# Kernel tuning notes

Hardware: AMD Instinct MI355X
Metric: run time of the kernel (lower is better)

Reference implementation:

```python
import jax, jax.numpy as jnp
import numpy as np

B, S, E, FF, Q = 8, 2048, 768, 3072, 8  # batch, seq, embed_dim, ffn_dim, n_qubits


def setup_inputs() -> dict:
    key = jax.random.key(0)
    k_x, k_phi, k_w1, k_w2 = jax.random.split(key, 4)
    x = jax.random.normal(k_x, (B, S, E), dtype=jnp.float32)
    # trainable RY angles (one per qubit), like tq.RY(has_params=True)
    phi = jax.random.normal(k_phi, (Q,), dtype=jnp.float32)
    # linear1: n_qubits -> ffn_dim ; linear2: ffn_dim -> embed_dim (torch layout [out, in])
    w1 = jax.random.normal(k_w1, (FF, Q), dtype=jnp.float32) / np.sqrt(Q).astype(np.float32)
    b1 = jnp.zeros((FF,), dtype=jnp.float32)
    w2 = jax.random.normal(k_w2, (E, FF), dtype=jnp.float32) / np.sqrt(FF).astype(np.float32)
    b2 = jnp.zeros((E,), dtype=jnp.float32)
    return {"x": x, "phi": phi, "w1": w1, "b1": b1, "w2": w2, "b2": b2}


def reference(x, phi, w1, b1, w2, b2):
    # Quantum block (exact closed form): for each token, encoder applies
    # RY(x_i) on wire i, then a trainable RY(phi_i) on wire i. Starting from
    # |0>^Q this is a product state; RY compose additively and
    # <Z> after RY(theta)|0> == cos(theta). MeasureAll(PauliZ) therefore gives:
    n_qubits = phi.shape[0]
    meas = jnp.cos(x[..., :n_qubits] + phi)          # [B, S, Q]
    # dropout is identity in eval mode
    h = jax.nn.relu(jnp.einsum('bsq,fq->bsf', meas, w1) + b1)  # [B, S, FF]
    return jnp.einsum('bsf,ef->bse', h, w2) + b2               # [B, S, E]
```

## Files before the change

kernel.cpp:

```cpp
#include <hip/hip_runtime.h>
#include <hip/hip_bf16.h>
#include <stdint.h>

#define M_TOK 16384
#define E_DIM 768
#define FF_DIM 3072
#define Q_N 8

typedef __attribute__((ext_vector_type(8))) short bf16x8;
typedef __attribute__((ext_vector_type(4))) float f32x4;

__device__ inline unsigned short f2bf(float f) {
  union { float f; unsigned u; } v; v.f = f;
  unsigned r = v.u + 0x7fffu + ((v.u >> 16) & 1u);
  return (unsigned short)(r >> 16);
}

__global__ __launch_bounds__(256) void cvt_w2(const float* __restrict__ w2,
                                              __hip_bfloat16* __restrict__ w2b) {
  int i = (blockIdx.x * 256 + threadIdx.x) * 4;
  const int n = E_DIM * FF_DIM;
  if (i < n) {
    float4 v = *(const float4*)(w2 + i);
    ushort4 o;
    o.x = f2bf(v.x); o.y = f2bf(v.y); o.z = f2bf(v.z); o.w = f2bf(v.w);
    *(ushort4*)((unsigned short*)w2b + i) = o;
  }
}

__global__ __launch_bounds__(256) void compute_h(const float* __restrict__ x,
                                                 const float* __restrict__ phi,
                                                 const float* __restrict__ w1,
                                                 const float* __restrict__ b1,
                                                 __hip_bfloat16* __restrict__ hout) {
  __shared__ float s_meas[32][8];
  const int t = threadIdx.x;
  const int bm = blockIdx.x / 6;
  const int bf = blockIdx.x % 6;
  const int m0 = bm * 32;
  const int f0 = bf * 512;

  if (t < 64) {
    int m = t >> 1, hh = t & 1;
    float4 v = *(const float4*)(x + (size_t)(m0 + m) * E_DIM + hh * 4);
    float4 p = *(const float4*)(phi + hh * 4);
    s_meas[m][hh * 4 + 0] = __cosf(v.x + p.x);
    s_meas[m][hh * 4 + 1] = __cosf(v.y + p.y);
    s_meas[m][hh * 4 + 2] = __cosf(v.z + p.z);
    s_meas[m][hh * 4 + 3] = __cosf(v.w + p.w);
  }
  __syncthreads();

  const float4* wr = (const float4*)(w1 + (size_t)(f0 + 2 * t) * Q_N);
  float4 a0 = wr[0], a1 = wr[1], b0 = wr[2], b1v = wr[3];
  float wA[8] = {a0.x, a0.y, a0.z, a0.w, a1.x, a1.y, a1.z, a1.w};
  float wB[8] = {b0.x, b0.y, b0.z, b0.w, b1v.x, b1v.y, b1v.z, b1v.w};
  const float biasA = b1[f0 + 2 * t];
  const float biasB = b1[f0 + 2 * t + 1];

  uint32_t* dst32 = (uint32_t*)hout;
  for (int m = 0; m < 32; ++m) {
    float a = biasA, b = biasB;
#pragma unroll
    for (int q = 0; q < 8; ++q) {
      float mv = s_meas[m][q];
      a = fmaf(mv, wA[q], a);
      b = fmaf(mv, wB[q], b);
    }
    a = fmaxf(a, 0.f);
    b = fmaxf(b, 0.f);
    uint32_t pack = (uint32_t)f2bf(a) | ((uint32_t)f2bf(b) << 16);
    dst32[(size_t)(m0 + m) * (FF_DIM / 2) + (f0 / 2) + t] = pack;
  }
}

#define GLDS16(g, l)                                                          \
  __builtin_amdgcn_global_load_lds(                                           \
      (const __attribute__((address_space(1))) void*)(g),                     \
      (__attribute__((address_space(3))) void*)(l), 16, 0, 0)

#define BUF_ELEMS 28672
#define B_OFF 16384

__global__ __launch_bounds__(512, 1) void gemm_bt(const __hip_bfloat16* __restrict__ A,
                                                  const __hip_bfloat16* __restrict__ Bw,
                                                  const float* __restrict__ b2,
                                                  float* __restrict__ C) {
  const int K = FF_DIM;
  const int N = E_DIM;

  __shared__ __align__(16) __hip_bfloat16 lds[2 * BUF_ELEMS];

  const int t = threadIdx.x;
  const int swz = (blockIdx.x & 7) * 32 + (blockIdx.x >> 3);
  const int bm = swz >> 2;
  const int bn = swz & 3;
  const size_t m0 = (size_t)bm * 256;
  const int n0 = bn * 192;

  const int w = t >> 6, l = t & 63;
  const int wr = w >> 2;
  const int wc = w & 3;
  const int lr = l & 15;
  const int lk = l >> 4;

  const int x0 = lk ^ (lr & 7);
  const int x1 = x0 ^ 4;
  const int baseA = (wr * 128 + lr) * 64;
  const int baseB = B_OFF + (wc * 48 + lr) * 64;
  const int offA0 = baseA + x0 * 8, offA1 = baseA + x1 * 8;
  const int offB0 = baseB + x0 * 8, offB1 = baseB + x1 * 8;

  const int rs = t >> 3;
  const int lc = (t & 7) ^ (rs & 7);
  const __hip_bfloat16* sA[4];
  const __hip_bfloat16* sB[3];
#pragma unroll
  for (int s = 0; s < 4; ++s) sA[s] = A + (m0 + s * 64 + rs) * (size_t)K + lc * 8;
#pragma unroll
  for (int s = 0; s < 3; ++s) sB[s] = Bw + ((size_t)n0 + s * 64 + rs) * K + lc * 8;

  f32x4 acc[8][3] = {};

#define S_EARLY(K0S, WBUF)                                                    \
  {                                                                           \
    __hip_bfloat16* ld = lds + (WBUF) * BUF_ELEMS + t * 8;                    \
    GLDS16(sB[0] + (K0S), ld + 16384);                                        \
    GLDS16(sB[1] + (K0S), ld + 20480);                                        \
    GLDS16(sB[2] + (K0S), ld + 24576);                                        \
    GLDS16(sA[0] + (K0S), ld);                                                \
    GLDS16(sA[2] + (K0S), ld + 8192);                                         \
  }
#define S_LATE(K0S, WBUF)                                                     \
  {                                                                           \
    __hip_bfloat16* ld = lds + (WBUF) * BUF_ELEMS + t * 8;                    \
    GLDS16(sA[1] + (K0S), ld + 4096);                                         \
    GLDS16(sA[3] + (K0S), ld + 12288);                                        \
  }

#define TILE(KT, RBUF, DO_STAGE)                                              \
  {                                                                           \
    const __hip_bfloat16* la = lds + (RBUF) * BUF_ELEMS;                      \
    if (DO_STAGE) S_EARLY(((KT) + 1) * 64, (RBUF) ^ 1);                       \
    bf16x8 af0[4], af1[4], bfx0[3], bfx1[3];                                  \
    _Pragma("unroll") for (int mi = 0; mi < 4; ++mi) {                        \
      af0[mi] = *(const bf16x8*)(la + offA0 + mi * 1024);                     \
      af1[mi] = *(const bf16x8*)(la + offA1 + mi * 1024);                     \
    }                                                                         \
    _Pragma("unroll") for (int ni = 0; ni < 3; ++ni) {                        \
      bfx0[ni] = *(const bf16x8*)(la + offB0 + ni * 1024);                    \
      bfx1[ni] = *(const bf16x8*)(la + offB1 + ni * 1024);                    \
    }                                                                         \
    __builtin_amdgcn_s_setprio(1);                                            \
    _Pragma("unroll") for (int mi = 0; mi < 4; ++mi)                          \
      _Pragma("unroll") for (int ni = 0; ni < 3; ++ni)                        \
        acc[mi][ni] = __builtin_amdgcn_mfma_f32_16x16x32_bf16(                \
            af0[mi], bfx0[ni], acc[mi][ni], 0, 0, 0);                         \
    _Pragma("unroll") for (int mi = 0; mi < 4; ++mi)                          \
      _Pragma("unroll") for (int ni = 0; ni < 3; ++ni)                        \
        acc[mi][ni] = __builtin_amdgcn_mfma_f32_16x16x32_bf16(                \
            af1[mi], bfx1[ni], acc[mi][ni], 0, 0, 0);                         \
    __builtin_amdgcn_s_setprio(0);                                            \
    if (DO_STAGE) {                                                           \
      asm volatile("s_waitcnt vmcnt(5)" ::: "memory");   \
    } else {                                                                  \
      asm volatile("s_waitcnt vmcnt(0)" ::: "memory");                        \
    }                                                                         \
    __builtin_amdgcn_s_barrier();                                             \
    bf16x8 ag0[4], ag1[4];                                                    \
    _Pragma("unroll") for (int mi = 0; mi < 4; ++mi) {                        \
      ag0[mi] = *(const bf16x8*)(la + offA0 + (mi + 4) * 1024);               \
      ag1[mi] = *(const bf16x8*)(la + offA1 + (mi + 4) * 1024);               \
    }                                                                         \
    if (DO_STAGE) S_LATE(((KT) + 1) * 64, (RBUF) ^ 1);                        \
    __builtin_amdgcn_s_setprio(1);                                            \
    _Pragma("unroll") for (int mi = 0; mi < 4; ++mi)                          \
      _Pragma("unroll") for (int ni = 0; ni < 3; ++ni)                        \
        acc[mi + 4][ni] = __builtin_amdgcn_mfma_f32_16x16x32_bf16(            \
            ag0[mi], bfx0[ni], acc[mi + 4][ni], 0, 0, 0);                     \
    _Pragma("unroll") for (int mi = 0; mi < 4; ++mi)                          \
      _Pragma("unroll") for (int ni = 0; ni < 3; ++ni)                        \
        acc[mi + 4][ni] = __builtin_amdgcn_mfma_f32_16x16x32_bf16(            \
            ag1[mi], bfx1[ni], acc[mi + 4][ni], 0, 0, 0);                     \
    __builtin_amdgcn_s_setprio(0);                                            \
    if (DO_STAGE) {                                                           \
      asm volatile("s_waitcnt vmcnt(2)" ::: "memory");  \
      __builtin_amdgcn_s_barrier();                                           \
    }                                                                         \
  }

  S_EARLY(0, 0);
  S_LATE(0, 0);
  asm volatile("s_waitcnt vmcnt(2)" ::: "memory");
  __builtin_amdgcn_s_barrier();

#pragma unroll 1
  for (int tt = 0; tt < 46; tt += 2) {
    TILE(tt + 0, 0, 1);
    TILE(tt + 1, 1, 1);
  }
  TILE(46, 0, 1);
  TILE(47, 1, 0);

#undef TILE
#undef S_EARLY
#undef S_LATE

#pragma unroll
  for (int mi = 0; mi < 8; ++mi) {
    const size_t row = m0 + wr * 128 + mi * 16 + lk * 4;
#pragma unroll
    for (int ni = 0; ni < 3; ++ni) {
      const int col = n0 + wc * 48 + ni * 16 + lr;
      const float bias = b2[col];
#pragma unroll
      for (int rr = 0; rr < 4; ++rr) {
        C[(row + rr) * N + col] = acc[mi][ni][rr] + bias;
      }
    }
  }
}

__global__ __launch_bounds__(256) void fallback_fused(const float* __restrict__ x,
                                                      const float* __restrict__ phi,
                                                      const float* __restrict__ w1,
                                                      const float* __restrict__ b1,
                                                      const float* __restrict__ w2,
                                                      const float* __restrict__ b2,
                                                      float* __restrict__ out) {
  __shared__ float s_h[FF_DIM];
  __shared__ float s_meas[Q_N];
  const int t = threadIdx.x;
  const size_t m = blockIdx.x;
  if (t < Q_N) s_meas[t] = __cosf(x[m * E_DIM + t] + phi[t]);
  __syncthreads();
  for (int f = t; f < FF_DIM; f += 256) {
    const float4* wr = (const float4*)(w1 + (size_t)f * Q_N);
    float4 a = wr[0], b = wr[1];
    float acc = b1[f];
    acc = fmaf(s_meas[0], a.x, acc); acc = fmaf(s_meas[1], a.y, acc);
    acc = fmaf(s_meas[2], a.z, acc); acc = fmaf(s_meas[3], a.w, acc);
    acc = fmaf(s_meas[4], b.x, acc); acc = fmaf(s_meas[5], b.y, acc);
    acc = fmaf(s_meas[6], b.z, acc); acc = fmaf(s_meas[7], b.w, acc);
    s_h[f] = fmaxf(acc, 0.f);
  }
  __syncthreads();
  for (int e = t; e < E_DIM; e += 256) {
    const float* w2r = w2 + (size_t)e * FF_DIM;
    float acc = b2[e];
    for (int f = 0; f < FF_DIM; f += 4) {
      float4 wv = *(const float4*)(w2r + f);
      acc = fmaf(s_h[f + 0], wv.x, acc);
      acc = fmaf(s_h[f + 1], wv.y, acc);
      acc = fmaf(s_h[f + 2], wv.z, acc);
      acc = fmaf(s_h[f + 3], wv.w, acc);
    }
    out[m * E_DIM + e] = acc;
  }
}

extern "C" void kernel_launch(void* const* d_in, const int* in_sizes, int n_in,
                              void* d_out, int out_size, void* d_ws, size_t ws_size,
                              hipStream_t stream) {
  const float* x   = (const float*)d_in[0];
  const float* phi = (const float*)d_in[1];
  const float* w1  = (const float*)d_in[2];
  const float* b1  = (const float*)d_in[3];
  const float* w2  = (const float*)d_in[4];
  const float* b2  = (const float*)d_in[5];
  float* out = (float*)d_out;

  const size_t H_BYTES   = (size_t)M_TOK * FF_DIM * 2;
  const size_t W2B_BYTES = (size_t)E_DIM * FF_DIM * 2;
  const size_t NEED = H_BYTES + W2B_BYTES;

  if (ws_size >= NEED) {
    __hip_bfloat16* h   = (__hip_bfloat16*)d_ws;
    __hip_bfloat16* w2b = (__hip_bfloat16*)((char*)d_ws + H_BYTES);
    cvt_w2<<<(E_DIM * FF_DIM) / (256 * 4), 256, 0, stream>>>(w2, w2b);
    compute_h<<<(M_TOK / 32) * (FF_DIM / 512), 256, 0, stream>>>(x, phi, w1, b1, h);
    gemm_bt<<<(M_TOK / 256) * (E_DIM / 192), 512, 0, stream>>>(h, w2b, b2, out);
  } else {
    fallback_fused<<<M_TOK, 256, 0, stream>>>(x, phi, w1, b1, w2, b2, out);
  }
}
```

Before: 99.91 us.

## Fuse hidden-layer computation into GEMM, generating A tiles in LDS on the fly

Drops the separate compute_h kernel and its 100MB bf16 hidden buffer. The GEMM kernel now computes cos(x+phi) per row once, streams w1/b1 slices into LDS, and computes each 256x64 A tile (FMA, ReLU, bf16 pack) straight into LDS while only B is fetched with global_load_lds. This removes the large HBM write and read of h and one kernel launch. In exchange each GEMM block recomputes h for its rows across 4 N-blocks, adds VALU work inside the main loop, and uses full vmcnt(0) waits instead of the finer split pipeline.

```diff
diff --git a/kernel.cpp b/kernel.cpp
--- a/kernel.cpp
+++ b/kernel.cpp
@@ -28,52 +28,6 @@
   }
 }
 
-__global__ __launch_bounds__(256) void compute_h(const float* __restrict__ x,
-                                                 const float* __restrict__ phi,
-                                                 const float* __restrict__ w1,
-                                                 const float* __restrict__ b1,
-                                                 __hip_bfloat16* __restrict__ hout) {
-  __shared__ float s_meas[32][8];
-  const int t = threadIdx.x;
-  const int bm = blockIdx.x / 6;
-  const int bf = blockIdx.x % 6;
-  const int m0 = bm * 32;
-  const int f0 = bf * 512;
-
-  if (t < 64) {
-    int m = t >> 1, hh = t & 1;
-    float4 v = *(const float4*)(x + (size_t)(m0 + m) * E_DIM + hh * 4);
-    float4 p = *(const float4*)(phi + hh * 4);
-    s_meas[m][hh * 4 + 0] = __cosf(v.x + p.x);
-    s_meas[m][hh * 4 + 1] = __cosf(v.y + p.y);
-    s_meas[m][hh * 4 + 2] = __cosf(v.z + p.z);
-    s_meas[m][hh * 4 + 3] = __cosf(v.w + p.w);
-  }
-  __syncthreads();
-
-  const float4* wr = (const float4*)(w1 + (size_t)(f0 + 2 * t) * Q_N);
-  float4 a0 = wr[0], a1 = wr[1], b0 = wr[2], b1v = wr[3];
-  float wA[8] = {a0.x, a0.y, a0.z, a0.w, a1.x, a1.y, a1.z, a1.w};
-  float wB[8] = {b0.x, b0.y, b0.z, b0.w, b1v.x, b1v.y, b1v.z, b1v.w};
-  const float biasA = b1[f0 + 2 * t];
-  const float biasB = b1[f0 + 2 * t + 1];
-
-  uint32_t* dst32 = (uint32_t*)hout;
-  for (int m = 0; m < 32; ++m) {
-    float a = biasA, b = biasB;
-#pragma unroll
-    for (int q = 0; q < 8; ++q) {
-      float mv = s_meas[m][q];
-      a = fmaf(mv, wA[q], a);
-      b = fmaf(mv, wB[q], b);
-    }
-    a = fmaxf(a, 0.f);
-    b = fmaxf(b, 0.f);
-    uint32_t pack = (uint32_t)f2bf(a) | ((uint32_t)f2bf(b) << 16);
-    dst32[(size_t)(m0 + m) * (FF_DIM / 2) + (f0 / 2) + t] = pack;
-  }
-}
-
 #define GLDS16(g, l)                                                          \
   __builtin_amdgcn_global_load_lds(                                           \
       (const __attribute__((address_space(1))) void*)(g),                     \
@@ -82,14 +36,19 @@
 #define BUF_ELEMS 28672
 #define B_OFF 16384
 
-__global__ __launch_bounds__(512, 1) void gemm_bt(const __hip_bfloat16* __restrict__ A,
-                                                  const __hip_bfloat16* __restrict__ Bw,
-                                                  const float* __restrict__ b2,
-                                                  float* __restrict__ C) {
+__global__ __launch_bounds__(512, 1) void ffn_fused(const float* __restrict__ x,
+                                                    const float* __restrict__ phi,
+                                                    const float* __restrict__ w1,
+                                                    const float* __restrict__ b1,
+                                                    const __hip_bfloat16* __restrict__ Bw,
+                                                    const float* __restrict__ b2,
+                                                    float* __restrict__ C) {
   const int K = FF_DIM;
   const int N = E_DIM;
 
   __shared__ __align__(16) __hip_bfloat16 lds[2 * BUF_ELEMS];
+  __shared__ __align__(16) float s_meas[256][8];
+  __shared__ __align__(16) float w1s[2][512];
 
   const int t = threadIdx.x;
   const int swz = (blockIdx.x & 7) * 32 + (blockIdx.x >> 3);
@@ -113,35 +72,94 @@
 
   const int rs = t >> 3;
   const int lc = (t & 7) ^ (rs & 7);
-  const __hip_bfloat16* sA[4];
   const __hip_bfloat16* sB[3];
 #pragma unroll
-  for (int s = 0; s < 4; ++s) sA[s] = A + (m0 + s * 64 + rs) * (size_t)K + lc * 8;
-#pragma unroll
   for (int s = 0; s < 3; ++s) sB[s] = Bw + ((size_t)n0 + s * 64 + rs) * K + lc * 8;
 
+  const int c4 = (((t >> 4) << 4) + ((t & 15) ^ ((t >> 4) & 7))) * 4;
+
   f32x4 acc[8][3] = {};
 
-#define S_EARLY(K0S, WBUF)                                                    \
+  {
+    const int m = t >> 1, hh = t & 1;
+    float4 v = *(const float4*)(x + (m0 + m) * (size_t)E_DIM + hh * 4);
+    float4 p = *(const float4*)(phi + hh * 4);
+    f32x4 cv;
+    cv[0] = __cosf(v.x + p.x); cv[1] = __cosf(v.y + p.y);
+    cv[2] = __cosf(v.z + p.z); cv[3] = __cosf(v.w + p.w);
+    *(f32x4*)&s_meas[m][hh * 4] = cv;
+  }
+  asm volatile("s_waitcnt lgkmcnt(0)" ::: "memory");
+  __builtin_amdgcn_s_barrier();
+
+  float mv[4][8];
+#pragma unroll
+  for (int s = 0; s < 4; ++s) {
+    f32x4 a = *(const f32x4*)&s_meas[rs + 64 * s][0];
+    f32x4 b = *(const f32x4*)&s_meas[rs + 64 * s][4];
+    mv[s][0] = a[0]; mv[s][1] = a[1]; mv[s][2] = a[2]; mv[s][3] = a[3];
+    mv[s][4] = b[0]; mv[s][5] = b[1]; mv[s][6] = b[2]; mv[s][7] = b[3];
+  }
+
+  if (t < 128) {
+    GLDS16(w1 + c4, (float*)w1s[0] + t * 4);
+    GLDS16(w1 + 512 + c4, (float*)w1s[1] + t * 4);
+  }
+  f32x4 b1a = *(const f32x4*)(b1 + lc * 8);
+  f32x4 b1b = *(const f32x4*)(b1 + lc * 8 + 4);
+
+  asm volatile("s_waitcnt vmcnt(0) lgkmcnt(0)" ::: "memory");
+  __builtin_amdgcn_s_barrier();
+
+#define HCOMP(WSEL, WBUF)                                                     \
+  {                                                                           \
+    const float* wbuf = w1s[(WSEL)];                                          \
+    __hip_bfloat16* ldh = lds + (WBUF) * BUF_ELEMS + t * 8;                   \
+    f32x4 wq[16];                                                             \
+    _Pragma("unroll") for (int jj = 0; jj < 16; ++jj)                         \
+        wq[jj] = *(const f32x4*)(wbuf + (lc * 16 + (jj ^ lc)) * 4);           \
+    _Pragma("unroll") for (int s = 0; s < 4; ++s) {                           \
+      uint32_t pk[4];                                                         \
+      _Pragma("unroll") for (int j = 0; j < 8; ++j) {                         \
+        float a = (j < 4) ? b1a[j] : b1b[j - 4];                              \
+        _Pragma("unroll") for (int q = 0; q < 8; ++q)                         \
+            a = fmaf(mv[s][q], wq[j * 2 + (q >> 2)][q & 3], a);               \
+        a = fmaxf(a, 0.f);                                                    \
+        unsigned short u = f2bf(a);                                           \
+        if (j & 1) pk[j >> 1] |= ((uint32_t)u) << 16;                         \
+        else pk[j >> 1] = (uint32_t)u;                                        \
+      }                                                                       \
+      uint4 pv; pv.x = pk[0]; pv.y = pk[1]; pv.z = pk[2]; pv.w = pk[3];       \
+      *(uint4*)(ldh + s * 4096) = pv;                                         \
+    }                                                                         \
+  }
+
+#define STAGE_B(K0S, WBUF)                                                    \
   {                                                                           \
     __hip_bfloat16* ld = lds + (WBUF) * BUF_ELEMS + t * 8;                    \
     GLDS16(sB[0] + (K0S), ld + 16384);                                        \
     GLDS16(sB[1] + (K0S), ld + 20480);                                        \
     GLDS16(sB[2] + (K0S), ld + 24576);                                        \
-    GLDS16(sA[0] + (K0S), ld);                                                \
-    GLDS16(sA[2] + (K0S), ld + 8192);                                         \
-  }
-#define S_LATE(K0S, WBUF)                                                     \
-  {                                                                           \
-    __hip_bfloat16* ld = lds + (WBUF) * BUF_ELEMS + t * 8;                    \
-    GLDS16(sA[1] + (K0S), ld + 4096);                                         \
-    GLDS16(sA[3] + (K0S), ld + 12288);                                        \
-  }
-
-#define TILE(KT, RBUF, DO_STAGE)                                              \
+  }
+
+  HCOMP(0, 0);
+  b1a = *(const f32x4*)(b1 + 64 + lc * 8);
+  b1b = *(const f32x4*)(b1 + 64 + lc * 8 + 4);
+  STAGE_B(0, 0);
+  asm volatile("s_waitcnt vmcnt(0) lgkmcnt(0)" ::: "memory");
+  __builtin_amdgcn_s_barrier();
+
+#define TILE(KT, RBUF, DO_AB, DO_W1)                                          \
   {                                                                           \
     const __hip_bfloat16* la = lds + (RBUF) * BUF_ELEMS;                      \
-    if (DO_STAGE) S_EARLY(((KT) + 1) * 64, (RBUF) ^ 1);                       \
+    if (DO_AB) STAGE_B(((KT) + 1) * 64, (RBUF) ^ 1);                          \
+    if (DO_AB) HCOMP(((KT) + 1) & 1, (RBUF) ^ 1);                             \
+    if (DO_W1) {                                                              \
+      if (t < 128) GLDS16(w1 + (size_t)((KT) + 2) * 512 + c4,                 \
+                          (float*)w1s[(KT) & 1] + t * 4);                     \
+      b1a = *(const f32x4*)(b1 + ((KT) + 2) * 64 + lc * 8);                   \
+      b1b = *(const f32x4*)(b1 + ((KT) + 2) * 64 + lc * 8 + 4);               \
+    }                                                                         \
     bf16x8 af0[4], af1[4], bfx0[3], bfx1[3];                                  \
     _Pragma("unroll") for (int mi = 0; mi < 4; ++mi) {                        \
       af0[mi] = *(const bf16x8*)(la + offA0 + mi * 1024);                     \
@@ -161,18 +179,11 @@
         acc[mi][ni] = __builtin_amdgcn_mfma_f32_16x16x32_bf16(                \
             af1[mi], bfx1[ni], acc[mi][ni], 0, 0, 0);                         \
     __builtin_amdgcn_s_setprio(0);                                            \
-    if (DO_STAGE) {                                                           \
-      asm volatile("s_waitcnt vmcnt(5)" ::: "memory");   \
-    } else {                                                                  \
-      asm volatile("s_waitcnt vmcnt(0)" ::: "memory");                        \
-    }                                                                         \
-    __builtin_amdgcn_s_barrier();                                             \
     bf16x8 ag0[4], ag1[4];                                                    \
     _Pragma("unroll") for (int mi = 0; mi < 4; ++mi) {                        \
       ag0[mi] = *(const bf16x8*)(la + offA0 + (mi + 4) * 1024);               \
       ag1[mi] = *(const bf16x8*)(la + offA1 + (mi + 4) * 1024);               \
     }                                                                         \
-    if (DO_STAGE) S_LATE(((KT) + 1) * 64, (RBUF) ^ 1);                        \
     __builtin_amdgcn_s_setprio(1);                                            \
     _Pragma("unroll") for (int mi = 0; mi < 4; ++mi)                          \
       _Pragma("unroll") for (int ni = 0; ni < 3; ++ni)                        \
@@ -183,28 +194,21 @@
         acc[mi + 4][ni] = __builtin_amdgcn_mfma_f32_16x16x32_bf16(            \
             ag1[mi], bfx1[ni], acc[mi + 4][ni], 0, 0, 0);                     \
     __builtin_amdgcn_s_setprio(0);                                            \
-    if (DO_STAGE) {                                                           \
-      asm volatile("s_waitcnt vmcnt(2)" ::: "memory");  \
-      __builtin_amdgcn_s_barrier();                                           \
-    }                                                                         \
-  }
-
-  S_EARLY(0, 0);
-  S_LATE(0, 0);
-  asm volatile("s_waitcnt vmcnt(2)" ::: "memory");
-  __builtin_amdgcn_s_barrier();
+    asm volatile("s_waitcnt vmcnt(0) lgkmcnt(0)" ::: "memory");               \
+    __builtin_amdgcn_s_barrier();                                             \
+  }
 
 #pragma unroll 1
   for (int tt = 0; tt < 46; tt += 2) {
-    TILE(tt + 0, 0, 1);
-    TILE(tt + 1, 1, 1);
-  }
-  TILE(46, 0, 1);
-  TILE(47, 1, 0);
+    TILE(tt + 0, 0, 1, 1);
+    TILE(tt + 1, 1, 1, 1);
+  }
+  TILE(46, 0, 1, 0);
+  TILE(47, 1, 0, 0);
 
 #undef TILE
-#undef S_EARLY
-#undef S_LATE
+#undef STAGE_B
+#undef HCOMP
 
 #pragma unroll
   for (int mi = 0; mi < 8; ++mi) {
@@ -270,16 +274,14 @@
   const float* b2  = (const float*)d_in[5];
   float* out = (float*)d_out;
 
-  const size_t H_BYTES   = (size_t)M_TOK * FF_DIM * 2;
   const size_t W2B_BYTES = (size_t)E_DIM * FF_DIM * 2;
-  const size_t NEED = H_BYTES + W2B_BYTES;
+  const size_t NEED = W2B_BYTES;
 
   if (ws_size >= NEED) {
-    __hip_bfloat16* h   = (__hip_bfloat16*)d_ws;
-    __hip_bfloat16* w2b = (__hip_bfloat16*)((char*)d_ws + H_BYTES);
+    __hip_bfloat16* w2b = (__hip_bfloat16*)d_ws;
     cvt_w2<<<(E_DIM * FF_DIM) / (256 * 4), 256, 0, stream>>>(w2, w2b);
-    compute_h<<<(M_TOK / 32) * (FF_DIM / 512), 256, 0, stream>>>(x, phi, w1, b1, h);
-    gemm_bt<<<(M_TOK / 256) * (E_DIM / 192), 512, 0, stream>>>(h, w2b, b2, out);
+    ffn_fused<<<(M_TOK / 256) * (E_DIM / 192), 512, 0, stream>>>(x, phi, w1, b1,
+                                                                 w2b, b2, out);
   } else {
     fallback_fused<<<M_TOK, 256, 0, stream>>>(x, phi, w1, b1, w2, b2, out);
   }
```

New measurement: 138.8 us. +39.0%, slower.
